# Performance work log

Measured on AMD Instinct MI355X. Metric: run time of the kernel, lower is better.

## Reference

```python
import jax, jax.numpy as jnp
import numpy as np

EMBED_DIM = 768
NUM_HEADS = 12
HEAD_DIM = EMBED_DIM // NUM_HEADS


def setup_inputs() -> dict:
    key = jax.random.key(0)
    k1, k2, k3, k4 = jax.random.split(key, 4)
    B, N, D = 8, 1024, EMBED_DIM
    x = jax.random.normal(k1, (B, N, D), dtype=jnp.float32)
    # qkv Linear (no bias): torch weight [3D, D]; we store transposed [D, 3D]
    W_qkv = jax.random.normal(k2, (D, 3 * D), dtype=jnp.float32) * (D ** -0.5)
    # projection Linear with bias
    W_proj = jax.random.normal(k3, (D, D), dtype=jnp.float32) * (D ** -0.5)
    b_proj = jax.random.normal(k4, (D,), dtype=jnp.float32) * 0.01
    return {"x": x, "W_qkv": W_qkv, "W_proj": W_proj, "b_proj": b_proj}


def reference(x, W_qkv, W_proj, b_proj):
    B, N, D = x.shape
    h, d = NUM_HEADS, HEAD_DIM
    scaling = d ** -0.5
    qkv = x @ W_qkv  # [B, N, 3D]
    # 'b n (qkv h d) -> qkv b h n d'
    qkv = qkv.reshape(B, N, 3, h, d).transpose(2, 0, 3, 1, 4)
    q, k, v = qkv[0], qkv[1], qkv[2]  # each [B, h, N, d]
    energy = jnp.einsum('bhid,bhjd->bhij', q, k) * scaling  # [B, h, N, N]
    att = jax.nn.softmax(energy, axis=-1)
    out = jnp.einsum('bhij,bhjd->bhid', att, v)  # [B, h, N, d]
    out = out.transpose(0, 2, 1, 3).reshape(B, N, D)  # 'b h n d -> b n (h d)'
    out = out @ W_proj + b_proj
    return out
```

## Files before the change

kernel.cpp:

```cpp
#include <hip/hip_runtime.h>
#include <hip/hip_bf16.h>

#define NUM_B 8
#define SEQ   1024
#define DIM   768
#define NH    12
#define HD    64

typedef __bf16 bf16x8 __attribute__((ext_vector_type(8)));
typedef float  f32x4  __attribute__((ext_vector_type(4)));

__device__ __forceinline__ unsigned short f2bf(float f) {
  unsigned int u = __float_as_uint(f);
  u += 0x7FFFu + ((u >> 16) & 1u);
  return (unsigned short)(u >> 16);
}

__global__ void cvt_kernel(const float* __restrict__ in, unsigned short* __restrict__ out, int n) {
  int i = (blockIdx.x * blockDim.x + threadIdx.x) * 4;
  if (i >= n) return;
  float4 v = *(const float4*)(in + i);
  ushort4 o = { f2bf(v.x), f2bf(v.y), f2bf(v.z), f2bf(v.w) };
  *(ushort4*)(out + i) = o;
}

__global__ void tcvt_kernel(const float* __restrict__ in, unsigned short* __restrict__ out,
                            int R, int C) {
  __shared__ unsigned short tile[32][33];
  int c0 = blockIdx.x * 32, r0 = blockIdx.y * 32;
  int tx = threadIdx.x, ty = threadIdx.y;
  #pragma unroll
  for (int i = 0; i < 32; i += 8)
    tile[ty + i][tx] = f2bf(in[(size_t)(r0 + ty + i) * C + c0 + tx]);
  __syncthreads();
  #pragma unroll
  for (int i = 0; i < 32; i += 8)
    out[(size_t)(c0 + ty + i) * R + r0 + tx] = tile[tx][ty + i];
}

template<bool QKV>
__global__ __launch_bounds__(256) void gemm_bf16(
    const unsigned short* __restrict__ A,
    const unsigned short* __restrict__ Bt,
    int K,
    unsigned short* __restrict__ qb,
    unsigned short* __restrict__ kb,
    unsigned short* __restrict__ vt,
    float* __restrict__ outp,
    const float* __restrict__ bias)
{
  __shared__ short As[128][40];
  __shared__ short Bs[128][40];
  const int m0 = blockIdx.x * 128, n0 = blockIdx.y * 128;
  const int t = threadIdx.x;
  const int lane = t & 63, w = t >> 6;
  const int l15 = lane & 15, g = lane >> 4;
  const int wm = w >> 1, wn = w & 1;
  const int ar = t >> 2, ac = (t & 3) * 8;

  f32x4 zv = {0.f, 0.f, 0.f, 0.f};
  f32x4 acc[4][4];
  #pragma unroll
  for (int i = 0; i < 4; ++i)
    #pragma unroll
    for (int j = 0; j < 4; ++j) acc[i][j] = zv;

  const size_t szK = (size_t)K;
  for (int k0 = 0; k0 < K; k0 += 32) {
    int4 a0 = *(const int4*)(A  + (size_t)(m0 + ar)      * szK + k0 + ac);
    int4 a1 = *(const int4*)(A  + (size_t)(m0 + ar + 64) * szK + k0 + ac);
    int4 b0 = *(const int4*)(Bt + (size_t)(n0 + ar)      * szK + k0 + ac);
    int4 b1 = *(const int4*)(Bt + (size_t)(n0 + ar + 64) * szK + k0 + ac);
    __syncthreads();
    *(int4*)&As[ar][ac]      = a0;
    *(int4*)&As[ar + 64][ac] = a1;
    *(int4*)&Bs[ar][ac]      = b0;
    *(int4*)&Bs[ar + 64][ac] = b1;
    __syncthreads();
    bf16x8 af[4], bfr[4];
    #pragma unroll
    for (int i = 0; i < 4; ++i) af[i]  = *(const bf16x8*)&As[wm*64 + i*16 + l15][g*8];
    #pragma unroll
    for (int i = 0; i < 4; ++i) bfr[i] = *(const bf16x8*)&Bs[wn*64 + i*16 + l15][g*8];
    #pragma unroll
    for (int i = 0; i < 4; ++i)
      #pragma unroll
      for (int j = 0; j < 4; ++j)
        acc[i][j] = __builtin_amdgcn_mfma_f32_16x16x32_bf16(af[i], bfr[j], acc[i][j], 0, 0, 0);
  }

  const int mbase = m0 + wm * 64, nbase = n0 + wn * 64;
  if (QKV) {
    #pragma unroll
    for (int i = 0; i < 4; ++i) {
      #pragma unroll
      for (int j = 0; j < 4; ++j) {
        int n = nbase + j * 16 + l15;
        int which = n / DIM;
        int jr = n - which * DIM;
        int head = jr >> 6, dd = jr & 63;
        size_t bhbase;
        #pragma unroll
        for (int r = 0; r < 4; ++r) {
          int m = mbase + i * 16 + g * 4 + r;
          int bb = m >> 10, nn = m & 1023;
          unsigned short val = f2bf(acc[i][j][r]);
          size_t bh = (size_t)bb * NH + head;
          if (which == 0)      qb[(bh * SEQ + nn) * HD + dd] = val;
          else if (which == 1) kb[(bh * SEQ + nn) * HD + dd] = val;
          else                 vt[(bh * HD + dd) * SEQ + nn] = val;
        }
        (void)bhbase;
      }
    }
  } else {
    #pragma unroll
    for (int i = 0; i < 4; ++i)
      #pragma unroll
      for (int j = 0; j < 4; ++j) {
        int n = nbase + j * 16 + l15;
        float bv = bias[n];
        #pragma unroll
        for (int r = 0; r < 4; ++r) {
          int m = mbase + i * 16 + g * 4 + r;
          outp[(size_t)m * DIM + n] = acc[i][j][r] + bv;
        }
      }
  }
}

__global__ __launch_bounds__(256) void attn_kernel(
    const unsigned short* __restrict__ qb,
    const unsigned short* __restrict__ kb,
    const unsigned short* __restrict__ vt,
    unsigned short* __restrict__ ao)
{
  __shared__ short Ks[64][72];
  __shared__ short Vs[64][72];
  __shared__ short Ps[4][32][72];
  const int bid = blockIdx.x;
  const int qt = (bid & 7) * 128;
  const int bh = bid >> 3;
  const int t = threadIdx.x, lane = t & 63, w = t >> 6;
  const int l15 = lane & 15, g = lane >> 4;
  const unsigned short* Qp = qb + (size_t)bh * SEQ * HD;
  const unsigned short* Kp = kb + (size_t)bh * SEQ * HD;
  const unsigned short* Vp = vt + (size_t)bh * HD * SEQ;
  const int q0 = qt + w * 32;

  bf16x8 aq[2][2];
  #pragma unroll
  for (int fm = 0; fm < 2; ++fm)
    #pragma unroll
    for (int kk = 0; kk < 2; ++kk)
      aq[fm][kk] = *(const bf16x8*)(Qp + (size_t)(q0 + fm*16 + l15) * HD + kk*32 + g*8);

  f32x4 zv = {0.f, 0.f, 0.f, 0.f};
  f32x4 accO[2][4];
  float mrow[2][4], lrow[2][4];
  #pragma unroll
  for (int fm = 0; fm < 2; ++fm) {
    #pragma unroll
    for (int j = 0; j < 4; ++j) accO[fm][j] = zv;
    #pragma unroll
    for (int r = 0; r < 4; ++r) { mrow[fm][r] = -INFINITY; lrow[fm][r] = 0.f; }
  }

  const int sr = t >> 3, sc = (t & 7) * 8;
  for (int kt = 0; kt < SEQ; kt += 64) {
    __syncthreads();
    *(int4*)&Ks[sr][sc]      = *(const int4*)(Kp + (size_t)(kt + sr)      * HD + sc);
    *(int4*)&Ks[sr + 32][sc] = *(const int4*)(Kp + (size_t)(kt + sr + 32) * HD + sc);
    *(int4*)&Vs[sr][sc]      = *(const int4*)(Vp + (size_t)sr        * SEQ + kt + sc);
    *(int4*)&Vs[sr + 32][sc] = *(const int4*)(Vp + (size_t)(sr + 32) * SEQ + kt + sc);
    __syncthreads();

    f32x4 s[2][4];
    #pragma unroll
    for (int fm = 0; fm < 2; ++fm)
      #pragma unroll
      for (int fn = 0; fn < 4; ++fn) s[fm][fn] = zv;
    #pragma unroll
    for (int fn = 0; fn < 4; ++fn)
      #pragma unroll
      for (int kk = 0; kk < 2; ++kk) {
        bf16x8 bk = *(const bf16x8*)&Ks[fn*16 + l15][kk*32 + g*8];
        s[0][fn] = __builtin_amdgcn_mfma_f32_16x16x32_bf16(aq[0][kk], bk, s[0][fn], 0, 0, 0);
        s[1][fn] = __builtin_amdgcn_mfma_f32_16x16x32_bf16(aq[1][kk], bk, s[1][fn], 0, 0, 0);
      }

    #pragma unroll
    for (int fm = 0; fm < 2; ++fm)
      #pragma unroll
      for (int r = 0; r < 4; ++r) {
        float s0 = s[fm][0][r] * 0.125f, s1 = s[fm][1][r] * 0.125f;
        float s2 = s[fm][2][r] * 0.125f, s3 = s[fm][3][r] * 0.125f;
        float mx = fmaxf(fmaxf(s0, s1), fmaxf(s2, s3));
        mx = fmaxf(mx, __shfl_xor(mx, 1, 64));
        mx = fmaxf(mx, __shfl_xor(mx, 2, 64));
        mx = fmaxf(mx, __shfl_xor(mx, 4, 64));
        mx = fmaxf(mx, __shfl_xor(mx, 8, 64));
        float mold = mrow[fm][r];
        float mnew = fmaxf(mold, mx);
        float al = __expf(mold - mnew);
        mrow[fm][r] = mnew;
        float p0 = __expf(s0 - mnew), p1 = __expf(s1 - mnew);
        float p2 = __expf(s2 - mnew), p3 = __expf(s3 - mnew);
        float rs = (p0 + p1) + (p2 + p3);
        rs += __shfl_xor(rs, 1, 64);
        rs += __shfl_xor(rs, 2, 64);
        rs += __shfl_xor(rs, 4, 64);
        rs += __shfl_xor(rs, 8, 64);
        lrow[fm][r] = lrow[fm][r] * al + rs;
        #pragma unroll
        for (int fn = 0; fn < 4; ++fn) accO[fm][fn][r] *= al;
        int prow = fm * 16 + g * 4 + r;
        Ps[w][prow][0*16 + l15] = (short)f2bf(p0);
        Ps[w][prow][1*16 + l15] = (short)f2bf(p1);
        Ps[w][prow][2*16 + l15] = (short)f2bf(p2);
        Ps[w][prow][3*16 + l15] = (short)f2bf(p3);
      }
    __syncthreads();

    bf16x8 ap[2][2];
    #pragma unroll
    for (int fm = 0; fm < 2; ++fm)
      #pragma unroll
      for (int kk = 0; kk < 2; ++kk)
        ap[fm][kk] = *(const bf16x8*)&Ps[w][fm*16 + l15][kk*32 + g*8];
    #pragma unroll
    for (int fn = 0; fn < 4; ++fn)
      #pragma unroll
      for (int kk = 0; kk < 2; ++kk) {
        bf16x8 bv = *(const bf16x8*)&Vs[fn*16 + l15][kk*32 + g*8];
        accO[0][fn] = __builtin_amdgcn_mfma_f32_16x16x32_bf16(ap[0][kk], bv, accO[0][fn], 0, 0, 0);
        accO[1][fn] = __builtin_amdgcn_mfma_f32_16x16x32_bf16(ap[1][kk], bv, accO[1][fn], 0, 0, 0);
      }
  }

  const int bb = bh / NH, hh = bh - bb * NH;
  #pragma unroll
  for (int fm = 0; fm < 2; ++fm)
    #pragma unroll
    for (int r = 0; r < 4; ++r) {
      float inv = 1.f / lrow[fm][r];
      int qq = q0 + fm * 16 + g * 4 + r;
      #pragma unroll
      for (int fn = 0; fn < 4; ++fn) {
        int dd = fn * 16 + l15;
        ao[((size_t)(bb * SEQ + qq)) * DIM + hh * HD + dd] = f2bf(accO[fm][fn][r] * inv);
      }
    }
}

extern "C" void kernel_launch(void* const* d_in, const int* in_sizes, int n_in,
                              void* d_out, int out_size, void* d_ws, size_t ws_size,
                              hipStream_t stream) {
  const float* x     = (const float*)d_in[0];
  const float* Wqkv  = (const float*)d_in[1];
  const float* Wproj = (const float*)d_in[2];
  const float* bproj = (const float*)d_in[3];
  float* out = (float*)d_out;

  unsigned short* ws = (unsigned short*)d_ws;
  const size_t NX = (size_t)NUM_B * SEQ * DIM;
  unsigned short* x_bf    = ws;
  unsigned short* Wqkv_t  = x_bf + NX;
  unsigned short* Wproj_t = Wqkv_t + (size_t)3 * DIM * DIM;
  unsigned short* qbuf    = Wproj_t + (size_t)DIM * DIM;
  unsigned short* kbuf    = qbuf + NX;
  unsigned short* vtb     = kbuf + NX;
  unsigned short* attb    = vtb + NX;

  cvt_kernel<<<dim3((unsigned)(NX / 4 / 256)), 256, 0, stream>>>(x, x_bf, (int)NX);
  tcvt_kernel<<<dim3(3 * DIM / 32, DIM / 32), dim3(32, 8), 0, stream>>>(Wqkv, Wqkv_t, DIM, 3 * DIM);
  tcvt_kernel<<<dim3(DIM / 32, DIM / 32), dim3(32, 8), 0, stream>>>(Wproj, Wproj_t, DIM, DIM);

  gemm_bf16<true><<<dim3(64, 18), 256, 0, stream>>>(
      x_bf, Wqkv_t, DIM, qbuf, kbuf, vtb, nullptr, nullptr);

  attn_kernel<<<dim3(NUM_B * NH * (SEQ / 128)), 256, 0, stream>>>(qbuf, kbuf, vtb, attb);

  gemm_bf16<false><<<dim3(64, 6), 256, 0, stream>>>(
      attb, Wproj_t, DIM, nullptr, nullptr, nullptr, out, bproj);
}
```

Before: 255.7 us.

## Compute transposed S=K·Qᵀ in registers, drop LDS staging, use exp2 with lazy rescale

Attention is restructured so each wave computes S transposed (K as the A operand, Q as B), which leaves each query's scores in one lane column. The P matrix can then be packed directly into MFMA B-operand registers, removing the shared-memory round trip for P and all __syncthreads. K and V are now read straight from global memory instead of being staged cooperatively through LDS. The softmax scale is folded together with log2(e) into Q in the QKV epilogue so exp2 can be used, and accumulator rescaling is skipped unless the row max grows by more than a threshold. The trade-off is redundant global/L2 reads of K and V across the four waves and narrower 8-byte V loads.

```diff
diff --git a/kernel.cpp b/kernel.cpp
--- a/kernel.cpp
+++ b/kernel.cpp
@@ -9,11 +9,26 @@
 
 typedef __bf16 bf16x8 __attribute__((ext_vector_type(8)));
 typedef float  f32x4  __attribute__((ext_vector_type(4)));
+typedef unsigned int u32;
+
+#define QSCL 0.18033688011112042f
 
 __device__ __forceinline__ unsigned short f2bf(float f) {
   unsigned int u = __float_as_uint(f);
   u += 0x7FFFu + ((u >> 16) & 1u);
   return (unsigned short)(u >> 16);
+}
+
+__device__ __forceinline__ float fexp2(float x) {
+#if __has_builtin(__builtin_amdgcn_exp2f)
+  return __builtin_amdgcn_exp2f(x);
+#else
+  return exp2f(x);
+#endif
+}
+
+__device__ __forceinline__ u32 pk2bf(float a, float b) {
+  return (u32)f2bf(a) | ((u32)f2bf(b) << 16);
 }
 
 __global__ void cvt_kernel(const float* __restrict__ in, unsigned short* __restrict__ out, int n) {
@@ -99,18 +114,17 @@
         int which = n / DIM;
         int jr = n - which * DIM;
         int head = jr >> 6, dd = jr & 63;
-        size_t bhbase;
+        float sc = (which == 0) ? QSCL : 1.0f;
         #pragma unroll
         for (int r = 0; r < 4; ++r) {
           int m = mbase + i * 16 + g * 4 + r;
           int bb = m >> 10, nn = m & 1023;
-          unsigned short val = f2bf(acc[i][j][r]);
+          unsigned short val = f2bf(acc[i][j][r] * sc);
           size_t bh = (size_t)bb * NH + head;
           if (which == 0)      qb[(bh * SEQ + nn) * HD + dd] = val;
           else if (which == 1) kb[(bh * SEQ + nn) * HD + dd] = val;
           else                 vt[(bh * HD + dd) * SEQ + nn] = val;
         }
-        (void)bhbase;
       }
     }
   } else {
@@ -135,9 +149,6 @@
     const unsigned short* __restrict__ vt,
     unsigned short* __restrict__ ao)
 {
-  __shared__ short Ks[64][72];
-  __shared__ short Vs[64][72];
-  __shared__ short Ps[4][32][72];
   const int bid = blockIdx.x;
   const int qt = (bid & 7) * 128;
   const int bh = bid >> 3;
@@ -148,109 +159,122 @@
   const unsigned short* Vp = vt + (size_t)bh * HD * SEQ;
   const int q0 = qt + w * 32;
 
-  bf16x8 aq[2][2];
-  #pragma unroll
-  for (int fm = 0; fm < 2; ++fm)
+  bf16x8 bq[2][2];
+  #pragma unroll
+  for (int nq = 0; nq < 2; ++nq)
     #pragma unroll
     for (int kk = 0; kk < 2; ++kk)
-      aq[fm][kk] = *(const bf16x8*)(Qp + (size_t)(q0 + fm*16 + l15) * HD + kk*32 + g*8);
+      bq[nq][kk] = *(const bf16x8*)(Qp + (size_t)(q0 + nq*16 + l15) * HD + kk*32 + g*8);
 
   f32x4 zv = {0.f, 0.f, 0.f, 0.f};
   f32x4 accO[2][4];
-  float mrow[2][4], lrow[2][4];
-  #pragma unroll
-  for (int fm = 0; fm < 2; ++fm) {
-    #pragma unroll
-    for (int j = 0; j < 4; ++j) accO[fm][j] = zv;
-    #pragma unroll
-    for (int r = 0; r < 4; ++r) { mrow[fm][r] = -INFINITY; lrow[fm][r] = 0.f; }
+  float m_[2] = { -INFINITY, -INFINITY };
+  float l_[2] = { 0.f, 0.f };
+  #pragma unroll
+  for (int nq = 0; nq < 2; ++nq)
+    #pragma unroll
+    for (int fn = 0; fn < 4; ++fn) accO[nq][fn] = zv;
+
+  for (int kt = 0; kt < SEQ; kt += 64) {
+    f32x4 s[2][4];
+    #pragma unroll
+    for (int nq = 0; nq < 2; ++nq)
+      #pragma unroll
+      for (int fm = 0; fm < 4; ++fm) s[nq][fm] = zv;
+    #pragma unroll
+    for (int fm = 0; fm < 4; ++fm)
+      #pragma unroll
+      for (int kk = 0; kk < 2; ++kk) {
+        bf16x8 ak = *(const bf16x8*)(Kp + (size_t)(kt + fm*16 + l15) * HD + kk*32 + g*8);
+        s[0][fm] = __builtin_amdgcn_mfma_f32_16x16x32_bf16(ak, bq[0][kk], s[0][fm], 0, 0, 0);
+        s[1][fm] = __builtin_amdgcn_mfma_f32_16x16x32_bf16(ak, bq[1][kk], s[1][fm], 0, 0, 0);
+      }
+
+    uint2 vl[4][2], vh[4][2];
+    #pragma unroll
+    for (int fn = 0; fn < 4; ++fn)
+      #pragma unroll
+      for (int cc = 0; cc < 2; ++cc) {
+        const unsigned short* vp = Vp + (size_t)(fn*16 + l15) * SEQ + kt + cc*32 + g*4;
+        vl[fn][cc] = *(const uint2*)(vp);
+        vh[fn][cc] = *(const uint2*)(vp + 16);
+      }
+
+    u32 bp[2][2][4];
+    #pragma unroll
+    for (int nq = 0; nq < 2; ++nq) {
+      f32x4 ma, mb, mc;
+      #pragma unroll
+      for (int r = 0; r < 4; ++r) {
+        ma[r] = fmaxf(s[nq][0][r], s[nq][1][r]);
+        mb[r] = fmaxf(s[nq][2][r], s[nq][3][r]);
+        mc[r] = fmaxf(ma[r], mb[r]);
+      }
+      float mx = fmaxf(fmaxf(mc[0], mc[1]), fmaxf(mc[2], mc[3]));
+      mx = fmaxf(mx, __shfl_xor(mx, 16, 64));
+      mx = fmaxf(mx, __shfl_xor(mx, 32, 64));
+      float mo = m_[nq];
+      if (__any(mx > mo + 11.0f)) {
+        float mn = fmaxf(mo, mx);
+        float al = fexp2(mo - mn);
+        m_[nq] = mn;
+        l_[nq] *= al;
+        #pragma unroll
+        for (int fn = 0; fn < 4; ++fn)
+          #pragma unroll
+          for (int r = 0; r < 4; ++r) accO[nq][fn][r] *= al;
+      }
+      float mn = m_[nq];
+      float p[4][4];
+      #pragma unroll
+      for (int fm = 0; fm < 4; ++fm)
+        #pragma unroll
+        for (int r = 0; r < 4; ++r)
+          p[fm][r] = fexp2(s[nq][fm][r] - mn);
+      float rs = ((p[0][0] + p[0][1]) + (p[0][2] + p[0][3]))
+               + ((p[1][0] + p[1][1]) + (p[1][2] + p[1][3]))
+               + ((p[2][0] + p[2][1]) + (p[2][2] + p[2][3]))
+               + ((p[3][0] + p[3][1]) + (p[3][2] + p[3][3]));
+      rs += __shfl_xor(rs, 16, 64);
+      rs += __shfl_xor(rs, 32, 64);
+      l_[nq] += rs;
+      #pragma unroll
+      for (int fm = 0; fm < 4; ++fm) {
+        int cc = fm >> 1, wi = (fm & 1) * 2;
+        bp[nq][cc][wi]     = pk2bf(p[fm][0], p[fm][1]);
+        bp[nq][cc][wi + 1] = pk2bf(p[fm][2], p[fm][3]);
+      }
+    }
+
+    #pragma unroll
+    for (int cc = 0; cc < 2; ++cc) {
+      union { u32 u[4]; bf16x8 v; } b0, b1;
+      #pragma unroll
+      for (int i = 0; i < 4; ++i) { b0.u[i] = bp[0][cc][i]; b1.u[i] = bp[1][cc][i]; }
+      #pragma unroll
+      for (int fn = 0; fn < 4; ++fn) {
+        union { u32 u[4]; bf16x8 v; } av;
+        av.u[0] = vl[fn][cc].x; av.u[1] = vl[fn][cc].y;
+        av.u[2] = vh[fn][cc].x; av.u[3] = vh[fn][cc].y;
+        accO[0][fn] = __builtin_amdgcn_mfma_f32_16x16x32_bf16(av.v, b0.v, accO[0][fn], 0, 0, 0);
+        accO[1][fn] = __builtin_amdgcn_mfma_f32_16x16x32_bf16(av.v, b1.v, accO[1][fn], 0, 0, 0);
+      }
+    }
   }
 
-  const int sr = t >> 3, sc = (t & 7) * 8;
-  for (int kt = 0; kt < SEQ; kt += 64) {
-    __syncthreads();
-    *(int4*)&Ks[sr][sc]      = *(const int4*)(Kp + (size_t)(kt + sr)      * HD + sc);
-    *(int4*)&Ks[sr + 32][sc] = *(const int4*)(Kp + (size_t)(kt + sr + 32) * HD + sc);
-    *(int4*)&Vs[sr][sc]      = *(const int4*)(Vp + (size_t)sr        * SEQ + kt + sc);
-    *(int4*)&Vs[sr + 32][sc] = *(const int4*)(Vp + (size_t)(sr + 32) * SEQ + kt + sc);
-    __syncthreads();
-
-    f32x4 s[2][4];
-    #pragma unroll
-    for (int fm = 0; fm < 2; ++fm)
-      #pragma unroll
-      for (int fn = 0; fn < 4; ++fn) s[fm][fn] = zv;
-    #pragma unroll
-    for (int fn = 0; fn < 4; ++fn)
-      #pragma unroll
-      for (int kk = 0; kk < 2; ++kk) {
-        bf16x8 bk = *(const bf16x8*)&Ks[fn*16 + l15][kk*32 + g*8];
-        s[0][fn] = __builtin_amdgcn_mfma_f32_16x16x32_bf16(aq[0][kk], bk, s[0][fn], 0, 0, 0);
-        s[1][fn] = __builtin_amdgcn_mfma_f32_16x16x32_bf16(aq[1][kk], bk, s[1][fn], 0, 0, 0);
-      }
-
-    #pragma unroll
-    for (int fm = 0; fm < 2; ++fm)
-      #pragma unroll
-      for (int r = 0; r < 4; ++r) {
-        float s0 = s[fm][0][r] * 0.125f, s1 = s[fm][1][r] * 0.125f;
-        float s2 = s[fm][2][r] * 0.125f, s3 = s[fm][3][r] * 0.125f;
-        float mx = fmaxf(fmaxf(s0, s1), fmaxf(s2, s3));
-        mx = fmaxf(mx, __shfl_xor(mx, 1, 64));
-        mx = fmaxf(mx, __shfl_xor(mx, 2, 64));
-        mx = fmaxf(mx, __shfl_xor(mx, 4, 64));
-        mx = fmaxf(mx, __shfl_xor(mx, 8, 64));
-        float mold = mrow[fm][r];
-        float mnew = fmaxf(mold, mx);
-        float al = __expf(mold - mnew);
-        mrow[fm][r] = mnew;
-        float p0 = __expf(s0 - mnew), p1 = __expf(s1 - mnew);
-        float p2 = __expf(s2 - mnew), p3 = __expf(s3 - mnew);
-        float rs = (p0 + p1) + (p2 + p3);
-        rs += __shfl_xor(rs, 1, 64);
-        rs += __shfl_xor(rs, 2, 64);
-        rs += __shfl_xor(rs, 4, 64);
-        rs += __shfl_xor(rs, 8, 64);
-        lrow[fm][r] = lrow[fm][r] * al + rs;
-        #pragma unroll
-        for (int fn = 0; fn < 4; ++fn) accO[fm][fn][r] *= al;
-        int prow = fm * 16 + g * 4 + r;
-        Ps[w][prow][0*16 + l15] = (short)f2bf(p0);
-        Ps[w][prow][1*16 + l15] = (short)f2bf(p1);
-        Ps[w][prow][2*16 + l15] = (short)f2bf(p2);
-        Ps[w][prow][3*16 + l15] = (short)f2bf(p3);
-      }
-    __syncthreads();
-
-    bf16x8 ap[2][2];
-    #pragma unroll
-    for (int fm = 0; fm < 2; ++fm)
-      #pragma unroll
-      for (int kk = 0; kk < 2; ++kk)
-        ap[fm][kk] = *(const bf16x8*)&Ps[w][fm*16 + l15][kk*32 + g*8];
-    #pragma unroll
-    for (int fn = 0; fn < 4; ++fn)
-      #pragma unroll
-      for (int kk = 0; kk < 2; ++kk) {
-        bf16x8 bv = *(const bf16x8*)&Vs[fn*16 + l15][kk*32 + g*8];
-        accO[0][fn] = __builtin_amdgcn_mfma_f32_16x16x32_bf16(ap[0][kk], bv, accO[0][fn], 0, 0, 0);
-        accO[1][fn] = __builtin_amdgcn_mfma_f32_16x16x32_bf16(ap[1][kk], bv, accO[1][fn], 0, 0, 0);
-      }
+  const int bb = bh / NH, hh = bh - bb * NH;
+  #pragma unroll
+  for (int nq = 0; nq < 2; ++nq) {
+    float inv = 1.0f / l_[nq];
+    int q = q0 + nq * 16 + l15;
+    unsigned short* op = ao + ((size_t)(bb * SEQ + q)) * DIM + hh * HD + g * 4;
+    #pragma unroll
+    for (int fn = 0; fn < 4; ++fn) {
+      ushort4 o = { f2bf(accO[nq][fn][0] * inv), f2bf(accO[nq][fn][1] * inv),
+                    f2bf(accO[nq][fn][2] * inv), f2bf(accO[nq][fn][3] * inv) };
+      *(ushort4*)(op + fn * 16) = o;
+    }
   }
-
-  const int bb = bh / NH, hh = bh - bb * NH;
-  #pragma unroll
-  for (int fm = 0; fm < 2; ++fm)
-    #pragma unroll
-    for (int r = 0; r < 4; ++r) {
-      float inv = 1.f / lrow[fm][r];
-      int qq = q0 + fm * 16 + g * 4 + r;
-      #pragma unroll
-      for (int fn = 0; fn < 4; ++fn) {
-        int dd = fn * 16 + l15;
-        ao[((size_t)(bb * SEQ + qq)) * DIM + hh * HD + dd] = f2bf(accO[fm][fn][r] * inv);
-      }
-    }
 }
 
 extern "C" void kernel_launch(void* const* d_in, const int* in_sizes, int n_in,
```

Measured after the change: 307.1 us. +20.1%, slower.
